# Kernel tuning notes

Hardware: AMD Instinct MI355X
Metric: run time of the kernel (lower is better)

## Reference

```python
import jax, jax.numpy as jnp
import numpy as np

NUM_HEADS = 16

def _rope(t, cos, sin):
    # t: [B,H,T,hd]; cos/sin: [T,half]
    half = t.shape[-1] // 2
    t1, t2 = t[..., :half], t[..., half:]
    return jnp.concatenate((t1 * cos - t2 * sin, t1 * sin + t2 * cos), axis=-1)

def setup_inputs() -> dict:
    key = jax.random.key(0)
    ks = jax.random.split(key, 5)
    B, T, D = 2, 2048, 2048
    s = 0.02
    return {
        'x': jax.random.normal(ks[0], (B, T, D), jnp.float32),
        'w_qkv': jax.random.normal(ks[1], (3 * D, D), jnp.float32) * s,
        'b_qkv': jax.random.normal(ks[2], (3 * D,), jnp.float32) * s,
        'w_out': jax.random.normal(ks[3], (D, D), jnp.float32) * s,
        'b_out': jax.random.normal(ks[4], (D,), jnp.float32) * s,
    }

def reference(x, w_qkv, b_qkv, w_out, b_out):
    B, T, D = x.shape
    H = NUM_HEADS
    hd = D // H
    half = hd // 2
    # fused QKV projection (torch Linear: x @ W^T + b)
    qkv = (x @ w_qkv.T + b_qkv).reshape(B, T, H, 3, hd)
    q, k, v = qkv[..., 0, :], qkv[..., 1, :], qkv[..., 2, :]
    q, k, v = (jnp.transpose(t, (0, 2, 1, 3)) for t in (q, k, v))  # [B,H,T,hd]
    # RoPE frequencies (buffer computed as in __init__)
    theta = 1.0 / (10000.0 ** (jnp.arange(half, dtype=jnp.float32) / half))
    freq = jnp.arange(T, dtype=jnp.float32)[:, None] * theta[None, :]  # [T,half]
    cos, sin = jnp.cos(freq), jnp.sin(freq)
    q = _rope(q, cos, sin)
    k = _rope(k, cos, sin)
    # causal attention; NOTE: source scales by embed_dim**-0.5
    scale = D ** (-0.5)
    scores = jnp.einsum('bhqd,bhkd->bhqk', q, k) * scale
    mask = jnp.triu(jnp.full((T, T), -1e9, dtype=scores.dtype), k=1)
    weights = jax.nn.softmax(scores + mask, axis=-1)
    attn = jnp.einsum('bhqk,bhkd->bhqd', weights, v)
    attn = jnp.transpose(attn, (0, 2, 1, 3)).reshape(B, T, D)
    return attn @ w_out.T + b_out
```

## Files before the change

### kernel.cpp

```cpp
#include <hip/hip_runtime.h>
#include <math.h>

#define NHEAD 16
#define TSEQ  2048
#define BATCH 2
#define DM    2048

typedef __attribute__((ext_vector_type(8))) short bf16x8;
typedef __attribute__((ext_vector_type(4))) float f32x4;

__device__ __forceinline__ short f2bf(float f) {
    unsigned u = __builtin_bit_cast(unsigned, f);
    u += 0x7fff + ((u >> 16) & 1);
    return (short)(u >> 16);
}
__device__ __forceinline__ float bf2f(short s) {
    unsigned u = ((unsigned)(unsigned short)s) << 16;
    return __builtin_bit_cast(float, u);
}
__device__ __forceinline__ void gload_lds16(const void* g, void* l) {
    __builtin_amdgcn_global_load_lds(
        (const __attribute__((address_space(1))) unsigned int*)g,
        (__attribute__((address_space(3))) unsigned int*)l, 16, 0, 0);
}

__global__ __launch_bounds__(256)
void cast_all(const float* __restrict__ x, short* __restrict__ xb,
              const float* __restrict__ wq, short* __restrict__ wqb,
              const float* __restrict__ wo, short* __restrict__ wob)
{
    int bid = blockIdx.x;
    const float* src; short* dst; int lb;
    if (bid < 4096)       { src = x;  dst = xb;  lb = bid; }
    else if (bid < 10240) { src = wq; dst = wqb; lb = bid - 4096; }
    else                  { src = wo; dst = wob; lb = bid - 10240; }
    int i = (lb * 256 + threadIdx.x) * 8;
    float4 a = *(const float4*)(src + i);
    float4 b = *(const float4*)(src + i + 4);
    bf16x8 o;
    o[0]=f2bf(a.x); o[1]=f2bf(a.y); o[2]=f2bf(a.z); o[3]=f2bf(a.w);
    o[4]=f2bf(b.x); o[5]=f2bf(b.y); o[6]=f2bf(b.z); o[7]=f2bf(b.w);
    *(bf16x8*)(dst + i) = o;
}

__global__ __launch_bounds__(256)
void gemm_qkv_rope(const short* __restrict__ A, const short* __restrict__ W,
                   const float* __restrict__ bias, short* __restrict__ qfrag,
                   short* __restrict__ kfrag, short* __restrict__ vfrag)
{
    const int K = 2048;
    __shared__ short sm[17408];
    short* As = sm;
    short* Bs = sm + 8192;
    const int tid = threadIdx.x;
    const int lane = tid & 63, w = tid >> 6;
    const int lane15 = lane & 15, quad = lane >> 4;
    const int wr = w >> 1, wc = w & 1;
    const int row0 = blockIdx.y * 128, col0 = blockIdx.x * 128;

    f32x4 acc[4][4];
    #pragma unroll
    for (int mi = 0; mi < 4; ++mi)
        #pragma unroll
        for (int ni = 0; ni < 4; ++ni)
            acc[mi][ni] = (f32x4){0.f, 0.f, 0.f, 0.f};

    for (int kt = 0; kt < K; kt += 64) {
        __syncthreads();
        #pragma unroll
        for (int i = 0; i < 4; ++i) {
            int ci = i * 256 + tid;
            int row = ci >> 3, lc = ci & 7;
            int gc = lc ^ (row & 7);
            gload_lds16(A + (size_t)(row0 + row) * K + kt + gc * 8, As + ci * 8);
            gload_lds16(W + (size_t)(col0 + row) * K + kt + gc * 8, Bs + ci * 8);
        }
        __syncthreads();
        #pragma unroll
        for (int kc = 0; kc < 2; ++kc) {
            bf16x8 af[4], bfr[4];
            #pragma unroll
            for (int mi = 0; mi < 4; ++mi) {
                int r = wr * 64 + mi * 16 + lane15;
                af[mi] = *(const bf16x8*)(As + r * 64 + ((kc * 4 + quad) ^ (r & 7)) * 8);
            }
            #pragma unroll
            for (int ni = 0; ni < 4; ++ni) {
                int r = wc * 64 + ni * 16 + lane15;
                bfr[ni] = *(const bf16x8*)(Bs + r * 64 + ((kc * 4 + quad) ^ (r & 7)) * 8);
            }
            #pragma unroll
            for (int mi = 0; mi < 4; ++mi)
                #pragma unroll
                for (int ni = 0; ni < 4; ++ni)
                    acc[mi][ni] = __builtin_amdgcn_mfma_f32_16x16x32_bf16(
                        af[mi], bfr[ni], acc[mi][ni], 0, 0, 0);
        }
    }

    const int head = col0 / 384;
    const int type = (col0 % 384) >> 7;
    const int b    = row0 >> 11;
    const int t0g  = row0 & 2047;
    const int bh   = b * NHEAD + head;

    __syncthreads();
    #pragma unroll
    for (int ni = 0; ni < 4; ++ni) {
        int d = wc * 64 + ni * 16 + lane15;
        float bv = bias[col0 + d];
        #pragma unroll
        for (int mi = 0; mi < 4; ++mi) {
            int rowb = wr * 64 + mi * 16 + quad * 4;
            #pragma unroll
            for (int r = 0; r < 4; ++r)
                sm[(rowb + r) * 136 + d] = f2bf(acc[mi][ni][r] + bv);
        }
    }
    __syncthreads();

    if (type < 2) {
        const float sc = (type == 0) ? 0.022097086912079608f : 1.0f;
        short* dst = (type == 0 ? qfrag : kfrag) + (size_t)bh * 262144;
        #pragma unroll
        for (int it = 0; it < 4; ++it) {
            int c = it * 256 + tid;
            int l15 = c & 15, q_ = (c >> 4) & 3, kc = (c >> 6) & 1, rowhi = c >> 7;
            int lrow = rowhi * 16 + l15;
            int t = t0g + lrow;
            bf16x8 a8 = *(const bf16x8*)(sm + lrow * 136 + kc * 32 + q_ * 8);
            bf16x8 b8 = *(const bf16x8*)(sm + lrow * 136 + kc * 32 + q_ * 8 + 64);
            bf16x8 oa, ob;
            #pragma unroll
            for (int j = 0; j < 8; ++j) {
                int d = kc * 32 + q_ * 8 + j;
                float trev = exp2f(-(float)d * (13.287712379549449f / 64.0f))
                             * 0.15915494309189535f;
                float ang = (float)t * trev;
                float fr = ang - floorf(ang);
                float sn, cs;
                __sincosf(fr * 6.283185307179586f, &sn, &cs);
                float va = bf2f(a8[j]), vb = bf2f(b8[j]);
                oa[j] = f2bf((va * cs - vb * sn) * sc);
                ob[j] = f2bf((va * sn + vb * cs) * sc);
            }
            size_t base = (size_t)((t0g >> 4) + rowhi) * 2048 + (q_ * 16 + l15) * 8;
            *(bf16x8*)(dst + base + kc * 512)        = oa;
            *(bf16x8*)(dst + base + kc * 512 + 1024) = ob;
        }
    } else {
        short* dst = vfrag + (size_t)bh * 262144;
        #pragma unroll
        for (int it = 0; it < 8; ++it) {
            int c = it * 256 + tid;
            int lane_ = c & 63, rest = c >> 6;
            int q_ = lane_ >> 4, l15 = lane_ & 15;
            int dt = rest & 7, kc2 = (rest >> 3) & 1, kbt = rest >> 4;
            int d = dt * 16 + l15;
            bf16x8 v;
            #pragma unroll
            for (int j = 0; j < 8; ++j)
                v[j] = sm[(kbt * 64 + kc2 * 32 + q_ * 8 + j) * 136 + d];
            *(bf16x8*)(dst + (size_t)((t0g >> 6) + kbt) * 8192
                        + dt * 1024 + kc2 * 512 + lane_ * 8) = v;
        }
    }
}

__global__ __launch_bounds__(256)
void gemm_out(const short* __restrict__ A, const short* __restrict__ W,
              const float* __restrict__ bias, float* __restrict__ Cout,
              int N, int K)
{
    __shared__ short As[128 * 64];
    __shared__ short Bs[128 * 64];
    const int tid = threadIdx.x;
    const int lane = tid & 63, w = tid >> 6;
    const int lane15 = lane & 15, quad = lane >> 4;
    const int wr = w >> 1, wc = w & 1;
    const int row0 = blockIdx.y * 128, col0 = blockIdx.x * 128;

    f32x4 acc[4][4];
    #pragma unroll
    for (int mi = 0; mi < 4; ++mi)
        #pragma unroll
        for (int ni = 0; ni < 4; ++ni)
            acc[mi][ni] = (f32x4){0.f, 0.f, 0.f, 0.f};

    for (int kt = 0; kt < K; kt += 64) {
        __syncthreads();
        #pragma unroll
        for (int i = 0; i < 4; ++i) {
            int ci = i * 256 + tid;
            int row = ci >> 3, lc = ci & 7;
            int gc = lc ^ (row & 7);
            gload_lds16(A + (size_t)(row0 + row) * K + kt + gc * 8, As + ci * 8);
            gload_lds16(W + (size_t)(col0 + row) * K + kt + gc * 8, Bs + ci * 8);
        }
        __syncthreads();
        #pragma unroll
        for (int kc = 0; kc < 2; ++kc) {
            bf16x8 af[4], bfr[4];
            #pragma unroll
            for (int mi = 0; mi < 4; ++mi) {
                int r = wr * 64 + mi * 16 + lane15;
                af[mi] = *(const bf16x8*)(As + r * 64 + ((kc * 4 + quad) ^ (r & 7)) * 8);
            }
            #pragma unroll
            for (int ni = 0; ni < 4; ++ni) {
                int r = wc * 64 + ni * 16 + lane15;
                bfr[ni] = *(const bf16x8*)(Bs + r * 64 + ((kc * 4 + quad) ^ (r & 7)) * 8);
            }
            #pragma unroll
            for (int mi = 0; mi < 4; ++mi)
                #pragma unroll
                for (int ni = 0; ni < 4; ++ni)
                    acc[mi][ni] = __builtin_amdgcn_mfma_f32_16x16x32_bf16(
                        af[mi], bfr[ni], acc[mi][ni], 0, 0, 0);
        }
    }

    #pragma unroll
    for (int mi = 0; mi < 4; ++mi)
        #pragma unroll
        for (int ni = 0; ni < 4; ++ni) {
            int col = col0 + wc * 64 + ni * 16 + lane15;
            float bv = bias[col];
            #pragma unroll
            for (int r = 0; r < 4; ++r) {
                int row = row0 + wr * 64 + mi * 16 + quad * 4 + r;
                Cout[(size_t)row * N + col] = acc[mi][ni][r] + bv;
            }
        }
}

__global__ __launch_bounds__(256)
void attn3(const short* __restrict__ qfrag, const short* __restrict__ kfrag,
           const short* __restrict__ vfrag, short* __restrict__ attnb)
{
    __shared__ short KV[2][16384];
    __shared__ short Pb[4][1152];
    const int tid = threadIdx.x;
    const int lane = tid & 63, w = tid >> 6;
    const int lane15 = lane & 15, quad = lane >> 4;
    const int g = (blockIdx.x + blockIdx.y) & 15;
    const int qb = blockIdx.z ? (15 - g) : g;
    const int h = blockIdx.y, b = blockIdx.z;
    const int bh = b * NHEAD + h;
    const int q0 = qb * 128;
    short* Pw = Pb[w];

    bf16x8 qf[2][4];
    {
        const short* qp = qfrag + (size_t)bh * 262144
                        + (size_t)(qb * 8 + w * 2) * 2048 + lane * 8;
        #pragma unroll
        for (int nq = 0; nq < 2; ++nq)
            #pragma unroll
            for (int kc = 0; kc < 4; ++kc)
                qf[nq][kc] = *(const bf16x8*)(qp + nq * 2048 + kc * 512);
    }

    f32x4 acc[8][2];
    #pragma unroll
    for (int dt = 0; dt < 8; ++dt)
        #pragma unroll
        for (int nq = 0; nq < 2; ++nq)
            acc[dt][nq] = (f32x4){0.f, 0.f, 0.f, 0.f};
    float m_s[2] = {-3e38f, -3e38f}, l_s[2] = {0.f, 0.f};

    const short* kf_src = kfrag + (size_t)bh * 262144;
    const short* vf_src = vfrag + (size_t)bh * 262144;
    const int kb_max = 2 * qb + 1;
    const int qtop = q0 + w * 32 + 31;
    const int diag0 = (q0 + w * 32) >> 6;

    #pragma unroll
    for (int i = 0; i < 4; ++i) {
        int ci = i * 256 + tid;
        gload_lds16(kf_src + ci * 8, KV[0] + ci * 8);
        gload_lds16(vf_src + ci * 8, KV[0] + 8192 + ci * 8);
    }

    for (int kb = 0; kb <= kb_max; ++kb) {
        __syncthreads();
        if (kb < kb_max) {
            const short* ks = kf_src + (size_t)(kb + 1) * 8192;
            const short* vs = vf_src + (size_t)(kb + 1) * 8192;
            short* kd = KV[(kb + 1) & 1];
            #pragma unroll
            for (int i = 0; i < 4; ++i) {
                int ci = i * 256 + tid;
                gload_lds16(ks + ci * 8, kd + ci * 8);
                gload_lds16(vs + ci * 8, kd + 8192 + ci * 8);
            }
        }
        if (kb * 64 > qtop) continue;
        const short* Ks = KV[kb & 1];
        const short* Vs = Ks + 8192;

        f32x4 st[2][4];
        #pragma unroll
        for (int nq = 0; nq < 2; ++nq)
            #pragma unroll
            for (int mi = 0; mi < 4; ++mi)
                st[nq][mi] = (f32x4){0.f, 0.f, 0.f, 0.f};
        #pragma unroll
        for (int mi = 0; mi < 4; ++mi) {
            bf16x8 kf4[4];
            #pragma unroll
            for (int kc = 0; kc < 4; ++kc)
                kf4[kc] = *(const bf16x8*)(Ks + ((mi * 4 + kc) * 64 + lane) * 8);
            #pragma unroll
            for (int kc = 0; kc < 4; ++kc)
                #pragma unroll
                for (int nq = 0; nq < 2; ++nq)
                    st[nq][mi] = __builtin_amdgcn_mfma_f32_16x16x32_bf16(
                        kf4[kc], qf[nq][kc], st[nq][mi], 0, 0, 0);
        }

        if (kb >= diag0) {
            #pragma unroll
            for (int nq = 0; nq < 2; ++nq) {
                int qg = q0 + w * 32 + nq * 16 + lane15;
                #pragma unroll
                for (int mi = 0; mi < 4; ++mi)
                    #pragma unroll
                    for (int r = 0; r < 4; ++r)
                        if (kb * 64 + mi * 16 + quad * 4 + r > qg)
                            st[nq][mi][r] = -3e38f;
            }
        }

        bf16x8 pb[2][2];
        #pragma unroll
        for (int nq = 0; nq < 2; ++nq) {
            float mt = st[nq][0][0];
            #pragma unroll
            for (int mi = 0; mi < 4; ++mi)
                #pragma unroll
                for (int r = 0; r < 4; ++r)
                    mt = fmaxf(mt, st[nq][mi][r]);
            mt = fmaxf(mt, __shfl_xor(mt, 16));
            mt = fmaxf(mt, __shfl_xor(mt, 32));
            float mn = fmaxf(m_s[nq], mt);
            float alpha = __expf(m_s[nq] - mn);
            m_s[nq] = mn;
            float sum = 0.f;
            #pragma unroll
            for (int mi = 0; mi < 4; ++mi)
                #pragma unroll
                for (int r = 0; r < 4; ++r) {
                    float p = __expf(st[nq][mi][r] - mn);
                    st[nq][mi][r] = p;
                    sum += p;
                }
            sum += __shfl_xor(sum, 16);
            sum += __shfl_xor(sum, 32);
            l_s[nq] = l_s[nq] * alpha + sum;
            #pragma unroll
            for (int dt = 0; dt < 8; ++dt) {
                acc[dt][nq][0] *= alpha; acc[dt][nq][1] *= alpha;
                acc[dt][nq][2] *= alpha; acc[dt][nq][3] *= alpha;
            }
            short* pr = Pw + lane15 * 72 + quad * 4;
            #pragma unroll
            for (int mi = 0; mi < 4; ++mi) {
                unsigned lo = (unsigned)(unsigned short)f2bf(st[nq][mi][0])
                            | ((unsigned)(unsigned short)f2bf(st[nq][mi][1]) << 16);
                unsigned hi = (unsigned)(unsigned short)f2bf(st[nq][mi][2])
                            | ((unsigned)(unsigned short)f2bf(st[nq][mi][3]) << 16);
                *(unsigned*)(pr + mi * 16)     = lo;
                *(unsigned*)(pr + mi * 16 + 2) = hi;
            }
            __asm__ volatile("s_waitcnt lgkmcnt(0)" ::: "memory");
            #pragma unroll
            for (int kc2 = 0; kc2 < 2; ++kc2)
                pb[nq][kc2] = *(const bf16x8*)(Pw + lane15 * 72 + kc2 * 32 + quad * 8);
            __asm__ volatile("s_waitcnt lgkmcnt(0)" ::: "memory");
        }

        #pragma unroll
        for (int dt = 0; dt < 8; ++dt)
            #pragma unroll
            for (int kc2 = 0; kc2 < 2; ++kc2) {
                bf16x8 vf = *(const bf16x8*)(Vs + ((dt * 2 + kc2) * 64 + lane) * 8);
                #pragma unroll
                for (int nq = 0; nq < 2; ++nq)
                    acc[dt][nq] = __builtin_amdgcn_mfma_f32_16x16x32_bf16(
                        vf, pb[nq][kc2], acc[dt][nq], 0, 0, 0);
            }
    }

    __syncthreads();
    short* Eb = KV[0];
    #pragma unroll
    for (int nq = 0; nq < 2; ++nq) {
        float inv = 1.f / l_s[nq];
        int qrow = w * 32 + nq * 16 + lane15;
        #pragma unroll
        for (int dt = 0; dt < 8; ++dt) {
            unsigned lo = (unsigned)(unsigned short)f2bf(acc[dt][nq][0] * inv)
                        | ((unsigned)(unsigned short)f2bf(acc[dt][nq][1] * inv) << 16);
            unsigned hi = (unsigned)(unsigned short)f2bf(acc[dt][nq][2] * inv)
                        | ((unsigned)(unsigned short)f2bf(acc[dt][nq][3] * inv) << 16);
            *(unsigned*)(Eb + qrow * 136 + dt * 16 + quad * 4)     = lo;
            *(unsigned*)(Eb + qrow * 136 + dt * 16 + quad * 4 + 2) = hi;
        }
    }
    __syncthreads();
    {
        int r = tid >> 1, half = tid & 1;
        short* orow = attnb + (size_t)(b * TSEQ + q0 + r) * DM + h * 128 + half * 64;
        #pragma unroll
        for (int i = 0; i < 8; ++i)
            *(bf16x8*)(orow + i * 8) =
                *(const bf16x8*)(Eb + r * 136 + half * 64 + i * 8);
    }
}

extern "C" void kernel_launch(void* const* d_in, const int* in_sizes, int n_in,
                              void* d_out, int out_size, void* d_ws, size_t ws_size,
                              hipStream_t stream)
{
    const float* x     = (const float*)d_in[0];
    const float* w_qkv = (const float*)d_in[1];
    const float* b_qkv = (const float*)d_in[2];
    const float* w_out = (const float*)d_in[3];
    const float* b_out = (const float*)d_in[4];
    float* out = (float*)d_out;

    char* ws = (char*)d_ws;
    short* xb    = (short*)(ws);
    short* wqkvb = (short*)(ws + 16777216);
    short* woutb = (short*)(ws + 41943040);
    short* qfrag = (short*)(ws + 50331648);
    short* kfrag = (short*)(ws + 67108864);
    short* vfrag = (short*)(ws + 83886080);
    short* attnb = xb;

    cast_all<<<12288, 256, 0, stream>>>(x, xb, w_qkv, wqkvb, w_out, woutb);

    {
        dim3 g2(48, 32);
        gemm_qkv_rope<<<g2, 256, 0, stream>>>(xb, wqkvb, b_qkv, qfrag, kfrag, vfrag);
    }
    {
        dim3 g2(16, NHEAD, BATCH);
        attn3<<<g2, 256, 0, stream>>>(qfrag, kfrag, vfrag, attnb);
    }
    {
        dim3 g2(16, 32);
        gemm_out<<<g2, 256, 0, stream>>>(attnb, woutb, b_out, out, 2048, 2048);
    }
}
```

Measured before the change: 382.9 us.

## Rewrite QKV GEMM as 256x256 tile with double-buffered ping-pong pipeline

The QKV projection GEMM moves from 128x128 tiles with 256 threads to 256x256 tiles with 512 threads and 128KB of double-buffered LDS. The K loop is split into quadrant MMA phases that overlap async global-to-LDS staging of the next K tiles with MFMA work, using explicit vmcnt/lgkmcnt waits, barriers and setprio. The epilogue now handles two 128-column head chunks per block. This targets global-load latency and raises data reuse per tile, at the cost of 64 accumulator registers per thread, only 384 blocks on the grid, and fragile hand-tuned synchronisation.

```diff
diff --git a/kernel.cpp b/kernel.cpp
--- a/kernel.cpp
+++ b/kernel.cpp
@@ -43,126 +43,210 @@
     *(bf16x8*)(dst + i) = o;
 }
 
-__global__ __launch_bounds__(256)
+#define BARRIER() __builtin_amdgcn_s_barrier()
+#define WAIT_LGKM0() do { asm volatile("s_waitcnt lgkmcnt(0)" ::: "memory"); \
+                          __builtin_amdgcn_sched_barrier(0); } while (0)
+#define WAIT_VM(N) asm volatile("s_waitcnt vmcnt(" #N ")" ::: "memory")
+
+#define LOAD_A(BUF, MH) do {                                                  \
+    const short* base_ = sm + (BUF)*32768 + (MH)*8192;                        \
+    _Pragma("unroll")                                                         \
+    for (int m_ = 0; m_ < 4; ++m_) {                                          \
+        int j_ = wr*64 + m_*16 + lane15;                                      \
+        const short* rp_ = base_ + j_*64;                                     \
+        int sw_ = (j_ & 7) << 3;                                              \
+        af[m_][0] = *(const bf16x8*)(rp_ + ((quad << 3) ^ sw_));              \
+        af[m_][1] = *(const bf16x8*)(rp_ + ((32 + (quad << 3)) ^ sw_));       \
+    }                                                                         \
+} while (0)
+
+#define LOAD_B(BUF, NH, BB) do {                                              \
+    const short* base_ = sm + (BUF)*32768 + 16384 + (NH)*8192;                \
+    _Pragma("unroll")                                                         \
+    for (int n_ = 0; n_ < 2; ++n_) {                                          \
+        int j_ = wc*32 + n_*16 + lane15;                                      \
+        const short* rp_ = base_ + j_*64;                                     \
+        int sw_ = (j_ & 7) << 3;                                              \
+        BB[n_][0] = *(const bf16x8*)(rp_ + ((quad << 3) ^ sw_));              \
+        BB[n_][1] = *(const bf16x8*)(rp_ + ((32 + (quad << 3)) ^ sw_));       \
+    }                                                                         \
+} while (0)
+
+#define STAGE_A(T, MH) do { if ((T) < 32) {                                   \
+    short* dst_ = sm + (((T) & 1) << 15) + ((MH) << 13);                      \
+    const int kt_ = (T) << 6;                                                 \
+    _Pragma("unroll")                                                         \
+    for (int i_ = 0; i_ < 2; ++i_) {                                          \
+        int ci_ = i_*512 + tid;                                               \
+        int j_ = ci_ >> 3, lc_ = ci_ & 7;                                     \
+        int r_ = (j_ & 63) + ((j_ >> 6) << 7) + (MH)*64;                      \
+        gload_lds16(A + (size_t)(row0 + r_)*2048 + kt_ + ((lc_ ^ (j_ & 7)) << 3), \
+                    dst_ + ci_*8);                                            \
+    } } } while (0)
+
+#define STAGE_B(T, NH) do { if ((T) < 32) {                                   \
+    short* dst_ = sm + (((T) & 1) << 15) + 16384 + ((NH) << 13);              \
+    const int kt_ = (T) << 6;                                                 \
+    _Pragma("unroll")                                                         \
+    for (int i_ = 0; i_ < 2; ++i_) {                                          \
+        int ci_ = i_*512 + tid;                                               \
+        int j_ = ci_ >> 3, lc_ = ci_ & 7;                                     \
+        int r_ = (j_ & 31) + ((j_ >> 5) << 6) + (NH)*32;                      \
+        gload_lds16(W + (size_t)(col0 + r_)*2048 + kt_ + ((lc_ ^ (j_ & 7)) << 3), \
+                    dst_ + ci_*8);                                            \
+    } } } while (0)
+
+#define MMA_Q(MH, NH, BB) do {                                                \
+    _Pragma("unroll")                                                         \
+    for (int m_ = 0; m_ < 4; ++m_) {                                          \
+        _Pragma("unroll")                                                     \
+        for (int n_ = 0; n_ < 2; ++n_) {                                      \
+            f32x4 c_ = acc[(MH)*4 + m_][(NH)*2 + n_];                         \
+            c_ = __builtin_amdgcn_mfma_f32_16x16x32_bf16(af[m_][0], BB[n_][0], c_, 0, 0, 0); \
+            c_ = __builtin_amdgcn_mfma_f32_16x16x32_bf16(af[m_][1], BB[n_][1], c_, 0, 0, 0); \
+            acc[(MH)*4 + m_][(NH)*2 + n_] = c_;                               \
+        }                                                                     \
+    }                                                                         \
+} while (0)
+
+__global__ __launch_bounds__(512, 2)
 void gemm_qkv_rope(const short* __restrict__ A, const short* __restrict__ W,
                    const float* __restrict__ bias, short* __restrict__ qfrag,
                    short* __restrict__ kfrag, short* __restrict__ vfrag)
 {
-    const int K = 2048;
-    __shared__ short sm[17408];
-    short* As = sm;
-    short* Bs = sm + 8192;
+    __shared__ short sm[65536];
     const int tid = threadIdx.x;
     const int lane = tid & 63, w = tid >> 6;
     const int lane15 = lane & 15, quad = lane >> 4;
-    const int wr = w >> 1, wc = w & 1;
-    const int row0 = blockIdx.y * 128, col0 = blockIdx.x * 128;
-
-    f32x4 acc[4][4];
-    #pragma unroll
-    for (int mi = 0; mi < 4; ++mi)
+    const int wr = w >> 2, wc = w & 3;
+    const int row0 = blockIdx.y * 256, col0 = blockIdx.x * 256;
+
+    f32x4 acc[8][4];
+    #pragma unroll
+    for (int mi = 0; mi < 8; ++mi)
         #pragma unroll
         for (int ni = 0; ni < 4; ++ni)
             acc[mi][ni] = (f32x4){0.f, 0.f, 0.f, 0.f};
 
-    for (int kt = 0; kt < K; kt += 64) {
+    bf16x8 af[4][2], bb0[2][2], bb1[2][2];
+
+    STAGE_A(0, 0); STAGE_B(0, 0); STAGE_A(0, 1); STAGE_B(0, 1);
+    STAGE_A(1, 0); STAGE_B(1, 0); STAGE_A(1, 1); STAGE_B(1, 1);
+    WAIT_VM(8);
+    BARRIER();
+
+    for (int i = 0; i < 16; ++i) {
+        const int ta = 2*i + 2;
+        const int tb = 2*i + 3;
+        LOAD_A(0, 0);
+        LOAD_B(0, 0, bb0);
+        BARRIER(); WAIT_LGKM0();
+        __builtin_amdgcn_s_setprio(1); MMA_Q(0, 0, bb0); __builtin_amdgcn_s_setprio(0);
+        BARRIER();
+        LOAD_B(0, 1, bb1);
+        STAGE_A(ta, 0); STAGE_B(ta, 0);
+        BARRIER(); WAIT_LGKM0();
+        __builtin_amdgcn_s_setprio(1); MMA_Q(0, 1, bb1); __builtin_amdgcn_s_setprio(0);
+        BARRIER();
+        LOAD_A(0, 1);
+        STAGE_B(ta, 1);
+        BARRIER(); WAIT_LGKM0();
+        __builtin_amdgcn_s_setprio(1); MMA_Q(1, 1, bb1); __builtin_amdgcn_s_setprio(0);
+        BARRIER();
+        STAGE_A(ta, 1);
+        if (i == 15) { WAIT_VM(0); } else { WAIT_VM(8); }
+        BARRIER();
+        __builtin_amdgcn_s_setprio(1); MMA_Q(1, 0, bb0); __builtin_amdgcn_s_setprio(0);
+        BARRIER();
+        LOAD_A(1, 0);
+        LOAD_B(1, 0, bb0);
+        BARRIER(); WAIT_LGKM0();
+        __builtin_amdgcn_s_setprio(1); MMA_Q(0, 0, bb0); __builtin_amdgcn_s_setprio(0);
+        BARRIER();
+        LOAD_B(1, 1, bb1);
+        STAGE_A(tb, 0); STAGE_B(tb, 0);
+        BARRIER(); WAIT_LGKM0();
+        __builtin_amdgcn_s_setprio(1); MMA_Q(0, 1, bb1); __builtin_amdgcn_s_setprio(0);
+        BARRIER();
+        LOAD_A(1, 1);
+        STAGE_B(tb, 1);
+        BARRIER(); WAIT_LGKM0();
+        __builtin_amdgcn_s_setprio(1); MMA_Q(1, 1, bb1); __builtin_amdgcn_s_setprio(0);
+        BARRIER();
+        STAGE_A(tb, 1);
+        if (i < 15) { WAIT_VM(8); }
+        BARRIER();
+        __builtin_amdgcn_s_setprio(1); MMA_Q(1, 0, bb0); __builtin_amdgcn_s_setprio(0);
+        BARRIER();
+    }
+
+    const int b = row0 >> 11;
+    const int t0g = row0 & 2047;
+    #pragma unroll
+    for (int ch = 0; ch < 2; ++ch) {
+        const int cidx = (col0 >> 7) + ch;
+        const int head = cidx / 3, type = cidx % 3;
         __syncthreads();
-        #pragma unroll
-        for (int i = 0; i < 4; ++i) {
-            int ci = i * 256 + tid;
-            int row = ci >> 3, lc = ci & 7;
-            int gc = lc ^ (row & 7);
-            gload_lds16(A + (size_t)(row0 + row) * K + kt + gc * 8, As + ci * 8);
-            gload_lds16(W + (size_t)(col0 + row) * K + kt + gc * 8, Bs + ci * 8);
+        if ((wc >> 1) == ch) {
+            #pragma unroll
+            for (int ni = 0; ni < 4; ++ni) {
+                int d = (wc & 1)*64 + ni*16 + lane15;
+                float bv = bias[col0 + ch*128 + d];
+                #pragma unroll
+                for (int mi = 0; mi < 8; ++mi) {
+                    int rowb = wr*128 + mi*16 + quad*4;
+                    #pragma unroll
+                    for (int r = 0; r < 4; ++r)
+                        sm[(rowb + r)*136 + d] = f2bf(acc[mi][ni][r] + bv);
+                }
+            }
         }
         __syncthreads();
-        #pragma unroll
-        for (int kc = 0; kc < 2; ++kc) {
-            bf16x8 af[4], bfr[4];
-            #pragma unroll
-            for (int mi = 0; mi < 4; ++mi) {
-                int r = wr * 64 + mi * 16 + lane15;
-                af[mi] = *(const bf16x8*)(As + r * 64 + ((kc * 4 + quad) ^ (r & 7)) * 8);
-            }
-            #pragma unroll
-            for (int ni = 0; ni < 4; ++ni) {
-                int r = wc * 64 + ni * 16 + lane15;
-                bfr[ni] = *(const bf16x8*)(Bs + r * 64 + ((kc * 4 + quad) ^ (r & 7)) * 8);
-            }
-            #pragma unroll
-            for (int mi = 0; mi < 4; ++mi)
-                #pragma unroll
-                for (int ni = 0; ni < 4; ++ni)
-                    acc[mi][ni] = __builtin_amdgcn_mfma_f32_16x16x32_bf16(
-                        af[mi], bfr[ni], acc[mi][ni], 0, 0, 0);
-        }
-    }
-
-    const int head = col0 / 384;
-    const int type = (col0 % 384) >> 7;
-    const int b    = row0 >> 11;
-    const int t0g  = row0 & 2047;
-    const int bh   = b * NHEAD + head;
-
-    __syncthreads();
-    #pragma unroll
-    for (int ni = 0; ni < 4; ++ni) {
-        int d = wc * 64 + ni * 16 + lane15;
-        float bv = bias[col0 + d];
-        #pragma unroll
-        for (int mi = 0; mi < 4; ++mi) {
-            int rowb = wr * 64 + mi * 16 + quad * 4;
-            #pragma unroll
-            for (int r = 0; r < 4; ++r)
-                sm[(rowb + r) * 136 + d] = f2bf(acc[mi][ni][r] + bv);
-        }
-    }
-    __syncthreads();
-
-    if (type < 2) {
-        const float sc = (type == 0) ? 0.022097086912079608f : 1.0f;
-        short* dst = (type == 0 ? qfrag : kfrag) + (size_t)bh * 262144;
-        #pragma unroll
-        for (int it = 0; it < 4; ++it) {
-            int c = it * 256 + tid;
-            int l15 = c & 15, q_ = (c >> 4) & 3, kc = (c >> 6) & 1, rowhi = c >> 7;
-            int lrow = rowhi * 16 + l15;
-            int t = t0g + lrow;
-            bf16x8 a8 = *(const bf16x8*)(sm + lrow * 136 + kc * 32 + q_ * 8);
-            bf16x8 b8 = *(const bf16x8*)(sm + lrow * 136 + kc * 32 + q_ * 8 + 64);
-            bf16x8 oa, ob;
-            #pragma unroll
-            for (int j = 0; j < 8; ++j) {
-                int d = kc * 32 + q_ * 8 + j;
-                float trev = exp2f(-(float)d * (13.287712379549449f / 64.0f))
-                             * 0.15915494309189535f;
-                float ang = (float)t * trev;
-                float fr = ang - floorf(ang);
-                float sn, cs;
-                __sincosf(fr * 6.283185307179586f, &sn, &cs);
-                float va = bf2f(a8[j]), vb = bf2f(b8[j]);
-                oa[j] = f2bf((va * cs - vb * sn) * sc);
-                ob[j] = f2bf((va * sn + vb * cs) * sc);
-            }
-            size_t base = (size_t)((t0g >> 4) + rowhi) * 2048 + (q_ * 16 + l15) * 8;
-            *(bf16x8*)(dst + base + kc * 512)        = oa;
-            *(bf16x8*)(dst + base + kc * 512 + 1024) = ob;
-        }
-    } else {
-        short* dst = vfrag + (size_t)bh * 262144;
-        #pragma unroll
-        for (int it = 0; it < 8; ++it) {
-            int c = it * 256 + tid;
-            int lane_ = c & 63, rest = c >> 6;
-            int q_ = lane_ >> 4, l15 = lane_ & 15;
-            int dt = rest & 7, kc2 = (rest >> 3) & 1, kbt = rest >> 4;
-            int d = dt * 16 + l15;
-            bf16x8 v;
-            #pragma unroll
-            for (int j = 0; j < 8; ++j)
-                v[j] = sm[(kbt * 64 + kc2 * 32 + q_ * 8 + j) * 136 + d];
-            *(bf16x8*)(dst + (size_t)((t0g >> 6) + kbt) * 8192
-                        + dt * 1024 + kc2 * 512 + lane_ * 8) = v;
+        if (type < 2) {
+            const float sc = (type == 0) ? 0.022097086912079608f : 1.0f;
+            short* dst = (type == 0 ? qfrag : kfrag) + (size_t)(b*NHEAD + head)*262144;
+            #pragma unroll
+            for (int it = 0; it < 4; ++it) {
+                int c = it*512 + tid;
+                int l15 = c & 15, q_ = (c >> 4) & 3, kc = (c >> 6) & 1, rowhi = c >> 7;
+                int lrow = rowhi*16 + l15;
+                int t = t0g + lrow;
+                bf16x8 a8 = *(const bf16x8*)(sm + lrow*136 + kc*32 + q_*8);
+                bf16x8 b8 = *(const bf16x8*)(sm + lrow*136 + kc*32 + q_*8 + 64);
+                bf16x8 oa, ob;
+                #pragma unroll
+                for (int j = 0; j < 8; ++j) {
+                    int d = kc*32 + q_*8 + j;
+                    float trev = exp2f(-(float)d * (13.287712379549449f / 64.0f))
+                                 * 0.15915494309189535f;
+                    float ang = (float)t * trev;
+                    float fr = ang - floorf(ang);
+                    float sn, cs;
+                    __sincosf(fr * 6.283185307179586f, &sn, &cs);
+                    float va = bf2f(a8[j]), vb = bf2f(b8[j]);
+                    oa[j] = f2bf((va*cs - vb*sn)*sc);
+                    ob[j] = f2bf((va*sn + vb*cs)*sc);
+                }
+                size_t base = (size_t)((t0g >> 4) + rowhi)*2048 + (q_*16 + l15)*8;
+                *(bf16x8*)(dst + base + kc*512)        = oa;
+                *(bf16x8*)(dst + base + kc*512 + 1024) = ob;
+            }
+        } else {
+            short* dst = vfrag + (size_t)(b*NHEAD + head)*262144;
+            #pragma unroll
+            for (int it = 0; it < 8; ++it) {
+                int c = it*512 + tid;
+                int lane_ = c & 63, rest = c >> 6;
+                int q_ = lane_ >> 4, l15 = lane_ & 15;
+                int dt = rest & 7, kc2 = (rest >> 3) & 1, kbt = rest >> 4;
+                int d = dt*16 + l15;
+                bf16x8 v;
+                #pragma unroll
+                for (int j = 0; j < 8; ++j)
+                    v[j] = sm[(kbt*64 + kc2*32 + q_*8 + j)*136 + d];
+                *(bf16x8*)(dst + (size_t)((t0g >> 6) + kbt)*8192
+                            + dt*1024 + kc2*512 + lane_*8) = v;
+            }
         }
     }
 }
@@ -442,8 +526,8 @@
     cast_all<<<12288, 256, 0, stream>>>(x, xb, w_qkv, wqkvb, w_out, woutb);
 
     {
-        dim3 g2(48, 32);
-        gemm_qkv_rope<<<g2, 256, 0, stream>>>(xb, wqkvb, b_qkv, qfrag, kfrag, vfrag);
+        dim3 g2(24, 16);
+        gemm_qkv_rope<<<g2, 512, 0, stream>>>(xb, wqkvb, b_qkv, qfrag, kfrag, vfrag);
     }
     {
         dim3 g2(16, NHEAD, BATCH);
```

Result: no change. 381.9 us (-0.3%).
